# Kernel tuning notes

Measured on AMD Instinct MI355X. Metric: run time of the kernel, lower is better.

Reference implementation:

```python
import jax, jax.numpy as jnp
import numpy as np

EPS = 1e-5  # BatchNorm eps (torch default)


def setup_inputs() -> dict:
    key = jax.random.key(0)
    ks = jax.random.split(key, 12)
    B, T, F = 2048, 128, 84

    def rn(k, sh, scale=0.05):
        return jax.random.normal(k, sh, jnp.float32) * scale

    return {
        "x": jax.random.normal(ks[0], (B, T, F), jnp.float32),
        # Conv1d(84 -> 64, k=3, pad=1)
        "conv1d_w": rn(ks[1], (64, F, 3)),
        "conv1d_b": rn(ks[2], (64,)),
        # BatchNorm1d(64), eval mode (running stats)
        "bn_gamma": jnp.ones((64,), jnp.float32),
        "bn_beta": jnp.zeros((64,), jnp.float32),
        "bn_mean": jnp.zeros((64,), jnp.float32),
        "bn_var": jnp.ones((64,), jnp.float32),
        # Linear(64*16 -> 64*4*4)
        "lin_w": rn(ks[3], (1024, 1024)),
        "lin_b": rn(ks[4], (1024,)),
        # ConvLSTM cell: Conv2d(192 -> 512, k=3, pad=1, groups=4)
        "cell_w": rn(ks[5], (512, 48, 3, 3)),
        "cell_b": rn(ks[6], (512,)),
        # Classifier
        "cls1_w": rn(ks[7], (128, 2048)),
        "cls1_b": rn(ks[8], (128,)),
        "cls2_w": rn(ks[9], (2, 128)),
        "cls2_b": rn(ks[10], (2,)),
    }


def reference(x, conv1d_w, conv1d_b, bn_gamma, bn_beta, bn_mean, bn_var,
              lin_w, lin_b, cell_w, cell_b, cls1_w, cls1_b, cls2_w, cls2_b):
    B, T, F = x.shape
    H = 128  # hidden channels

    # Per-timestep encoder is state-free -> vectorize over (B, T).
    # Conv1d k=3 pad=1 on a length-1 sequence: only the center tap hits data.
    enc = jnp.einsum('btf,cf->btc', x, conv1d_w[:, :, 1]) + conv1d_b  # [B,T,64]
    enc = (enc - bn_mean) * (bn_gamma / jnp.sqrt(bn_var + EPS)) + bn_beta
    enc = jax.nn.relu(enc)
    # flatten of [64,16] is channel-major -> repeat along last axis.
    flat = jnp.repeat(enc, 16, axis=-1)                               # [B,T,1024]
    to2d = jnp.einsum('btk,ok->bto', flat, lin_w) + lin_b             # [B,T,1024]
    xt = to2d.reshape(B, T, 64, 4, 4).transpose(1, 0, 2, 3, 4)        # [T,B,64,4,4]

    def step(carry, x_t):
        h, c = carry
        comb = jnp.concatenate([x_t, h], axis=1)                      # [B,192,4,4]
        conv = jax.lax.conv_general_dilated(
            comb, cell_w, window_strides=(1, 1), padding='SAME',
            dimension_numbers=('NCHW', 'OIHW', 'NCHW'),
            feature_group_count=4)
        conv = conv + cell_b[None, :, None, None]                     # [B,512,4,4]
        cc_i, cc_f, cc_o, cc_g = jnp.split(conv, 4, axis=1)
        c_next = jax.nn.sigmoid(cc_f) * c + jax.nn.sigmoid(cc_i) * jnp.tanh(cc_g)
        h_next = jax.nn.sigmoid(cc_o) * jnp.tanh(c_next)
        return (h_next, c_next), None

    h0 = jnp.zeros((B, H, 4, 4), x.dtype)
    (h_last, _), _ = jax.lax.scan(step, (h0, h0), xt)

    feat = h_last.reshape(B, H * 16)                                  # [B,2048]
    hid = jax.nn.relu(feat @ cls1_w.T + cls1_b)
    return hid @ cls2_w.T + cls2_b                                    # [B,2]
```

## Files before the change

kernel.cpp:

```cpp
#include <hip/hip_runtime.h>
#include <math.h>

#define BN_EPS 1e-5f

typedef _Float16 f16x8 __attribute__((ext_vector_type(8)));
typedef _Float16 f16x4 __attribute__((ext_vector_type(4)));
typedef _Float16 f16x2 __attribute__((ext_vector_type(2)));
typedef unsigned short u16x8 __attribute__((ext_vector_type(8)));
typedef float f32x4 __attribute__((ext_vector_type(4)));
typedef float f32x16 __attribute__((ext_vector_type(16)));


__global__ void prep_enc_w(const float* __restrict__ conv1d_w,
                           const float* __restrict__ conv1d_b,
                           const float* __restrict__ gamma,
                           const float* __restrict__ beta,
                           const float* __restrict__ mean,
                           const float* __restrict__ var,
                           float* __restrict__ We, float* __restrict__ be) {
  int tid = blockIdx.x * blockDim.x + threadIdx.x;
  if (tid < 5376) {
    int c = tid / 84, f = tid % 84;
    float s = gamma[c] * rsqrtf(var[c] + BN_EPS);
    We[c * 84 + f] = s * conv1d_w[c * 252 + f * 3 + 1];
    if (f == 0) be[c] = s * conv1d_b[c] + (beta[c] - mean[c] * s);
  }
}

__global__ void prep_wef(const float* __restrict__ We, _Float16* __restrict__ WeF) {
  int tid = blockIdx.x * blockDim.x + threadIdx.x;
  if (tid >= 6144) return;
  int j = tid & 7, lane = (tid >> 3) & 63, kch = (tid >> 9) % 3, ct = tid / 1536;
  int c = ct * 16 + (lane & 15);
  int k = kch * 32 + (lane >> 4) * 8 + j;
  WeF[tid] = (k < 84) ? (_Float16)We[c * 84 + k] : (_Float16)0.f;
}

__global__ void prep_w2(const float* __restrict__ lin_w, float* __restrict__ W2) {
  int tid = blockIdx.x * blockDim.x + threadIdx.x;
  int o2 = tid >> 6, c = tid & 63;
  float s = 0.f;
#pragma unroll
  for (int j = 0; j < 16; ++j) s += lin_w[o2 * 1024 + c * 16 + j];
  W2[o2 * 64 + c] = s;
}

__global__ void prep_A(const float* __restrict__ cell_w,
                       const float* __restrict__ cell_b,
                       const float* __restrict__ lin_b,
                       const float* __restrict__ W2,
                       float* __restrict__ A, float* __restrict__ Abias) {
  int tid = blockIdx.x * blockDim.x + threadIdx.x;
  int go = tid >> 10;
  int c = (tid >> 4) & 63;
  int p = tid & 15;
  int y = p >> 2, x = p & 3;
  int kn = (go >= 128) ? 16 : 48;
  int xb = (go >= 128) ? 48 : 0;
  float a = 0.f;
  for (int k = 0; k < kn; ++k)
    for (int dy = 0; dy < 3; ++dy) {
      int yy = y + dy - 1;
      if (yy < 0 || yy > 3) continue;
      for (int dx = 0; dx < 3; ++dx) {
        int xx = x + dx - 1;
        if (xx < 0 || xx > 3) continue;
        a += cell_w[((go * 48 + k) * 3 + dy) * 3 + dx] *
             W2[((xb + k) * 16 + yy * 4 + xx) * 64 + c];
      }
    }
  A[(go * 64 + c) * 16 + p] = a;
  if (c == 0) {
    float bs = cell_b[go];
    for (int k = 0; k < kn; ++k)
      for (int dy = 0; dy < 3; ++dy) {
        int yy = y + dy - 1;
        if (yy < 0 || yy > 3) continue;
        for (int dx = 0; dx < 3; ++dx) {
          int xx = x + dx - 1;
          if (xx < 0 || xx > 3) continue;
          bs += cell_w[((go * 48 + k) * 3 + dy) * 3 + dx] *
                lin_b[(xb + k) * 16 + yy * 4 + xx];
        }
      }
    Abias[go * 16 + p] = bs;
  }
}

__global__ void pack_a16(const float* __restrict__ A, _Float16* __restrict__ Apk) {
  int tid = blockIdx.x * blockDim.x + threadIdx.x;
  int j = tid & 7, lane = (tid >> 3) & 63, kch = (tid >> 9) & 1, go = tid >> 10;
  int p = lane & 15;
  int c = kch * 32 + (lane >> 4) * 8 + j;
  Apk[tid] = (_Float16)A[(go * 64 + c) * 16 + p];
}

__global__ void pack_wcv(const float* __restrict__ cell_w, _Float16* __restrict__ Wcv) {
  int tid = blockIdx.x * blockDim.x + threadIdx.x;
  int j = tid & 7, lane = (tid >> 3) & 63, m = (tid >> 9) & 3, tmk = tid >> 11;
  int co = m * 32 + (lane & 31);
  int khi = (lane >> 5) * 8 + j;
  float v;
  if (tmk < 18) {
    int kch = tmk / 9, tap = tmk % 9;
    v = cell_w[((size_t)(128 + co) * 48 + 16 + kch * 16 + khi) * 9 + tap];
  } else if (tmk < 45) {
    int r = tmk - 18; int kch = r / 9, tap = r % 9;
    v = cell_w[((size_t)(256 + co) * 48 + kch * 16 + khi) * 9 + tap];
  } else {
    int r = tmk - 45; int kch = r / 9, tap = r % 9;
    v = cell_w[((size_t)(384 + co) * 48 + kch * 16 + khi) * 9 + tap];
  }
  Wcv[tid] = (_Float16)v;
}

__device__ __forceinline__ float sigm(float v) {
  return __fdividef(1.f, 1.f + __expf(-v));
}
__device__ __forceinline__ float tanh_fast(float v) {
  return 1.f - __fdividef(2.f, __expf(2.f * v) + 1.f);
}

__global__ __launch_bounds__(256, 3) void xgate_kernel(
    const float* __restrict__ x, const _Float16* __restrict__ WeF,
    const float* __restrict__ be, const _Float16* __restrict__ Apk,
    const float* __restrict__ Abias, unsigned short* __restrict__ sixf, int tc) {
  __shared__ __align__(16) _Float16 x16[128 * 104];
  __shared__ __align__(16) _Float16 enc_s[128 * 72];
  __shared__ __align__(16) unsigned char Tt[4 * 2304];
  int tid = threadIdx.x, lane = tid & 63, w = tid >> 6;
  int gq = blockIdx.x >> 7, cq = blockIdx.x & 127;
  int n = lane & 15, kgrp = lane >> 4;

  {
    int r = tid >> 1, half = tid & 1;
    int b = cq * 16 + (r >> 3), t = tc * 8 + (r & 7);
    const float* rowp = x + ((size_t)b * 128 + t) * 84;
#pragma unroll
    for (int j = 0; j < 11; ++j) {
      int q = half + 2 * j;
      if (q < 21) {
        float4 v = *(const float4*)(rowp + q * 4);
        f16x4 h;
        h[0] = (_Float16)v.x; h[1] = (_Float16)v.y;
        h[2] = (_Float16)v.z; h[3] = (_Float16)v.w;
        *(f16x4*)(&x16[r * 104 + q * 4]) = h;
      }
    }
    for (int i = tid; i < 4096; i += 256) {
      int rr = i >> 5, k = i & 31;
      if (k < 20) x16[rr * 104 + 84 + k] = (_Float16)0.f;
    }
  }
  __syncthreads();

  for (int ct4 = 0; ct4 < 8; ++ct4) {
    f32x4 acc = *(const f32x4*)(be + w * 16 + kgrp * 4);
#pragma unroll
    for (int kch = 0; kch < 3; ++kch)
      acc = __builtin_amdgcn_mfma_f32_16x16x32_f16(
          *(const f16x8*)(WeF + ((w * 3 + kch) * 64 + lane) * 8),
          *(const f16x8*)(&x16[(ct4 * 16 + n) * 104 + kch * 32 + kgrp * 8]),
          acc, 0, 0, 0);
#pragma unroll
    for (int r = 0; r < 4; ++r)
      enc_s[(ct4 * 16 + n) * 72 + w * 16 + kgrp * 4 + r] =
          (_Float16)fmaxf(acc[r], 0.f);
  }
  __syncthreads();

  int slotB = gq >> 1;
  int chbase = (gq & 1) * 64 + w * 16;
  unsigned char* Tw = Tt + w * 2304;
  int fn = lane >> 2;
  for (int ct4 = 0; ct4 < 8; ++ct4) {
    int ccl = ct4 * 16 + n;
    int fb = cq * 16 + ct4 * 2 + (fn >> 3), ftr = fn & 7;
    size_t grow =
        (((size_t)fb * 8 + ftr) * 2 + slotB) * 2048 + (size_t)chbase * 16;
    for (int gb = 0; gb < 4; ++gb) {
#pragma unroll
      for (int gi = 0; gi < 4; ++gi) {
        int gol = gb * 4 + gi;
        int go = gq * 64 + w * 16 + gol;
        f32x4 acc = *(const f32x4*)(Abias + go * 16 + kgrp * 4);
        acc = __builtin_amdgcn_mfma_f32_16x16x32_f16(
            *(const f16x8*)(Apk + (size_t)go * 1024 + lane * 8),
            *(const f16x8*)(&enc_s[ccl * 72 + kgrp * 8]), acc, 0, 0, 0);
        acc = __builtin_amdgcn_mfma_f32_16x16x32_f16(
            *(const f16x8*)(Apk + (size_t)go * 1024 + 512 + lane * 8),
            *(const f16x8*)(&enc_s[ccl * 72 + 32 + kgrp * 8]), acc, 0, 0, 0);
        unsigned char* tdst = Tw + n * 144 + gi * 32 + kgrp * 8;
        if (gq < 2) {
#pragma unroll
          for (int rp = 0; rp < 2; ++rp) {
            unsigned lo = (unsigned)(sigm(acc[rp * 2]) * 65535.f + 0.5f);
            unsigned hi = (unsigned)(sigm(acc[rp * 2 + 1]) * 65535.f + 0.5f);
            *(unsigned*)(tdst + rp * 4) = lo | (hi << 16);
          }
        } else {
#pragma unroll
          for (int rp = 0; rp < 2; ++rp) {
            f16x2 pv = {(_Float16)acc[rp * 2], (_Float16)acc[rp * 2 + 1]};
            *(f16x2*)(tdst + rp * 4) = pv;
          }
        }
      }
      asm volatile("s_waitcnt lgkmcnt(0)" ::: "memory");
      __builtin_amdgcn_sched_barrier(0);
#pragma unroll
      for (int j = 0; j < 2; ++j) {
        int chunk = (lane & 3) + 4 * j;
        f16x8 v = *(const f16x8*)(Tw + fn * 144 + chunk * 16);
        *(f16x8*)(sixf + grow + (size_t)gb * 64 + (size_t)chunk * 8) = v;
      }
      asm volatile("s_waitcnt lgkmcnt(0)" ::: "memory");
      __builtin_amdgcn_sched_barrier(0);
    }
  }
}

#define HPB 4624
#define HPQ 272
#define ZQ 4352
#define COFF 36992
#define GOFF 102528
#define GSZ 18432
#define CBOFF 157824
#define LDSZ 158848

__device__ __forceinline__ void update_items(
    unsigned char* lds, const unsigned short* __restrict__ sixf_b,
    _Float16* __restrict__ h16_b, int tid, int q) {
  int tP = q >> 2, hfP = (q >> 1) & 1, ntP = q & 1;
  bool lastT = (tP == 7);
  float* cbase = (float*)(lds + COFF) + (hfP * 2 + ntP) * 4096;
#pragma unroll 2
  for (int k = 0; k < 6; ++k) {
    int item = tid + k * 768;
    if (item < 4096) {
      int cell = item >> 4, p = item & 15;
      int ch = cell & 127, blbit = cell >> 7;
      int b = hfP * 4 + ntP * 2 + blbit;
      const unsigned short* sp =
          sixf_b + ((size_t)b * 8 + tP) * 4096 + ch * 16 + p;
      float si = (float)sp[0] * (1.f / 65535.f);
      float xf = (float)*(const _Float16*)(sp + 2048);
      unsigned gbyte = (unsigned)(ch * 144 + ntP * 64 + blbit * 32 + p * 2);
      float gf = (float)*(const _Float16*)(lds + GOFF + 0 * GSZ + gbyte);
      float go = (float)*(const _Float16*)(lds + GOFF + 1 * GSZ + gbyte);
      float gg = (float)*(const _Float16*)(lds + GOFF + 2 * GSZ + gbyte);
      float cbo = *(const float*)(lds + CBOFF + ch * 4);
      float cbg = *(const float*)(lds + CBOFF + 512 + ch * 4);
      float* cp = cbase + cell * 16 + p;
      float cv = sigm(xf + gf) * cp[0] + si * tanh_fast(cbg + gg);
      cp[0] = cv;
      float hn = sigm(cbo + go) * tanh_fast(cv);
      *(_Float16*)(lds + b * HPB + p * HPQ + ch * 2) = (_Float16)hn;
      if (lastT) h16_b[((size_t)b * 16 + p) * 128 + ch] = (_Float16)hn;
    }
  }
}

template <int GATE>
__device__ __forceinline__ void role_loop(
    unsigned char* lds, const _Float16* __restrict__ Wg,
    const unsigned short* __restrict__ sixf_b,
    _Float16* __restrict__ h16_b,
    int m, int lane, int tid, const unsigned* tapbase, unsigned gwbase) {
  constexpr int NKCH = (GATE == 0) ? 2 : 3;
  constexpr unsigned CIOFF = (GATE == 0) ? 0u : (GATE == 1 ? 64u : 160u);
  f16x8 wr[NKCH * 9];
#pragma unroll
  for (int fi = 0; fi < NKCH * 9; ++fi)
    wr[fi] = *(const f16x8*)(Wg + (size_t)(fi * 4 + m) * 512 + (lane << 3));

  for (int q = 0; q < 32; ++q) {
    if (q > 0) update_items(lds, sixf_b, h16_b, tid, q - 1);
    int hf = (q >> 1) & 1, nt = q & 1;
    unsigned bofs = (unsigned)(hf * 4 + nt * 2) * HPB;
    f32x16 acc = {};
#pragma unroll
    for (int kch = 0; kch < NKCH; ++kch)
#pragma unroll
      for (int tap = 0; tap < 9; ++tap)
        acc = __builtin_amdgcn_mfma_f32_32x32x16_f16(
            wr[kch * 9 + tap],
            *(const f16x8*)(lds + tapbase[tap] + bofs + CIOFF +
                            (unsigned)kch * 32),
            acc, 0, 0, 0);
#pragma unroll
    for (int r = 0; r < 16; ++r) {
      unsigned co_l = (unsigned)((r & 3) + 8 * (r >> 2));
      *(_Float16*)(lds + gwbase + (unsigned)GATE * GSZ + co_l * 144u +
                   (unsigned)nt * 64u) = (_Float16)acc[r];
    }
    __syncthreads();
  }
  update_items(lds, sixf_b, h16_b, tid, 31);
  __syncthreads();
}

__global__ __launch_bounds__(768, 3) void recur8_kernel(
    const unsigned short* __restrict__ sixf, const _Float16* __restrict__ Wcv,
    const float* __restrict__ cell_b, _Float16* __restrict__ h16,
    float* __restrict__ cstate) {
  __shared__ __align__(16) unsigned char lds[LDSZ];
  int tid = threadIdx.x, lane = tid & 63, w = tid >> 6;
  int gate = w >> 2, m = w & 3;

  _Float16* h16_b = h16 + (size_t)blockIdx.x * 16384;
  for (int i = tid; i < 16384; i += 768) {
    int bl8 = i >> 11, q = (i >> 7) & 15, chh = i & 127;
    *(_Float16*)(lds + bl8 * HPB + q * HPQ + chh * 2) = h16_b[i];
  }
  for (int i = tid; i < 1024; i += 768) {
    int bl8 = i >> 7, chh = i & 127;
    *(_Float16*)(lds + bl8 * HPB + ZQ + chh * 2) = (_Float16)0.f;
  }
  float* cl = (float*)(lds + COFF);
  float* cst_b = cstate + (size_t)blockIdx.x * 16384;
  for (int i = tid; i < 16384; i += 768) cl[i] = cst_b[i];
  if (tid < 256) *(float*)(lds + CBOFF + tid * 4) = cell_b[256 + tid];

  int col = lane & 31, khalf = lane >> 5, b_lo = col >> 4, p_c = col & 15;
  int yc = p_c >> 2, xc = p_c & 3;
  unsigned tapbase[9];
#pragma unroll
  for (int dy = 0; dy < 3; ++dy)
#pragma unroll
    for (int dx = 0; dx < 3; ++dx) {
      int qy = yc + dy - 1, qx = xc + dx - 1;
      bool valid = (qy >= 0 && qy < 4 && qx >= 0 && qx < 4);
      tapbase[dy * 3 + dx] =
          (valid ? (unsigned)((qy * 4 + qx) * HPQ) : (unsigned)ZQ) +
          (unsigned)(b_lo * HPB + khalf * 16);
    }
  unsigned gwbase = (unsigned)GOFF + (unsigned)((m * 32 + khalf * 4) * 144) +
                    (unsigned)(b_lo * 32 + p_c * 2);
  __syncthreads();

  const unsigned short* sixf_b = sixf + (size_t)blockIdx.x * 262144;
  if (gate == 0)
    role_loop<0>(lds, Wcv, sixf_b, h16_b, m, lane, tid, tapbase, gwbase);
  else if (gate == 1)
    role_loop<1>(lds, Wcv + 36864, sixf_b, h16_b, m, lane, tid, tapbase, gwbase);
  else
    role_loop<2>(lds, Wcv + 92160, sixf_b, h16_b, m, lane, tid, tapbase, gwbase);

  for (int i = tid; i < 16384; i += 768) cst_b[i] = cl[i];
}

__global__ __launch_bounds__(128) void cls_kernel(
    const _Float16* __restrict__ h16, const float* __restrict__ w1,
    const float* __restrict__ b1, const float* __restrict__ w2,
    const float* __restrict__ b2, float* __restrict__ out) {
  __shared__ __align__(16) float feat[8 * 2064];
  __shared__ float hid[8 * 128];
  int b0 = blockIdx.x * 8;
  for (int i = threadIdx.x; i < 16384; i += 128) {
    int bl = i >> 11, r = i & 2047, p = r >> 7, chh = r & 127;
    feat[bl * 2064 + chh * 16 + p] = (float)h16[(size_t)b0 * 2048 + i];
  }
  __syncthreads();
  int ch = threadIdx.x;
  float acc[8];
#pragma unroll
  for (int b = 0; b < 8; ++b) acc[b] = b1[ch];
  const float4* wr = (const float4*)(w1 + (size_t)ch * 2048);
  for (int k4 = 0; k4 < 512; ++k4) {
    float4 wv = wr[k4];
#pragma unroll
    for (int b = 0; b < 8; ++b) {
      float4 f = *(const float4*)(&feat[b * 2064 + k4 * 4]);
      acc[b] += wv.x * f.x + wv.y * f.y + wv.z * f.z + wv.w * f.w;
    }
  }
#pragma unroll
  for (int b = 0; b < 8; ++b) hid[b * 128 + ch] = fmaxf(acc[b], 0.f);
  __syncthreads();
  if (threadIdx.x < 16) {
    int b = threadIdx.x >> 1, o = threadIdx.x & 1;
    float s = b2[o];
    for (int k = 0; k < 128; ++k) s += hid[b * 128 + k] * w2[o * 128 + k];
    out[(size_t)(b0 + b) * 2 + o] = s;
  }
}

extern "C" void kernel_launch(void* const* d_in, const int* in_sizes, int n_in,
                              void* d_out, int out_size, void* d_ws, size_t ws_size,
                              hipStream_t stream) {
  const float* x        = (const float*)d_in[0];
  const float* conv1d_w = (const float*)d_in[1];
  const float* conv1d_b = (const float*)d_in[2];
  const float* bn_gamma = (const float*)d_in[3];
  const float* bn_beta  = (const float*)d_in[4];
  const float* bn_mean  = (const float*)d_in[5];
  const float* bn_var   = (const float*)d_in[6];
  const float* lin_w    = (const float*)d_in[7];
  const float* lin_b    = (const float*)d_in[8];
  const float* cell_w   = (const float*)d_in[9];
  const float* cell_b   = (const float*)d_in[10];
  const float* cls1_w   = (const float*)d_in[11];
  const float* cls1_b   = (const float*)d_in[12];
  const float* cls2_w   = (const float*)d_in[13];
  const float* cls2_b   = (const float*)d_in[14];

  float* ws = (float*)d_ws;
  float* We    = ws + 0;
  float* be    = ws + 8192;
  float* W2    = ws + 12288;
  float* A     = ws + 81920;
  float* Abias = ws + 344064;
  _Float16* WeF = (_Float16*)(ws + 348160);
  _Float16* Apk = (_Float16*)(ws + 352256);
  _Float16* Wcv = (_Float16*)(ws + 483328);
  _Float16* h16 = (_Float16*)(ws + 557056);
  float* cstate = ws + 2654208;
  unsigned short* sixf = (unsigned short*)(ws + 6848512);
  float* out = (float*)d_out;

  prep_enc_w<<<21, 256, 0, stream>>>(conv1d_w, conv1d_b, bn_gamma, bn_beta,
                                     bn_mean, bn_var, We, be);
  prep_wef<<<24, 256, 0, stream>>>(We, WeF);
  prep_w2<<<256, 256, 0, stream>>>(lin_w, W2);
  prep_A<<<1024, 256, 0, stream>>>(cell_w, cell_b, lin_b, W2, A, Abias);
  pack_a16<<<1024, 256, 0, stream>>>(A, Apk);
  pack_wcv<<<576, 256, 0, stream>>>(cell_w, Wcv);
  hipMemsetAsync(h16, 0, 8388608, stream);
  hipMemsetAsync(cstate, 0, 16777216, stream);
  for (int tc = 0; tc < 16; ++tc) {
    xgate_kernel<<<512, 256, 0, stream>>>(x, WeF, be, Apk, Abias, sixf, tc);
    recur8_kernel<<<256, 768, 0, stream>>>(sixf, Wcv, cell_b, h16, cstate);
  }
  cls_kernel<<<256, 128, 0, stream>>>(h16, cls1_w, cls1_b, cls2_w, cls2_b, out);
}
```

Baseline: 3.651 ms.

## Vectorize LSTM cell update and assign fixed per-thread update tasks by warp role

Replaces the strided per-element gate update loop with a per-thread task that processes 8 spatial positions using 16-byte vector loads from global and LDS. Each thread keeps a fixed channel/batch-bit/half assignment, and the cell biases live in registers instead of LDS. The work is split across the gate roles: gate-0 warps update every step, while gate-1 and gate-2 warps alternate by tile parity. This cuts the address arithmetic, scalar loads and bias LDS traffic in the update phase. In exchange, the update work is spread unevenly across the warp roles and register pressure rises.

```diff
diff --git a/kernel.cpp b/kernel.cpp
--- a/kernel.cpp
+++ b/kernel.cpp
@@ -226,39 +226,35 @@
 #define COFF 36992
 #define GOFF 102528
 #define GSZ 18432
-#define CBOFF 157824
-#define LDSZ 158848
-
-__device__ __forceinline__ void update_items(
+#define LDSZ 157824
+
+__device__ __forceinline__ void vupdate(
     unsigned char* lds, const unsigned short* __restrict__ sixf_b,
-    _Float16* __restrict__ h16_b, int tid, int q) {
+    _Float16* __restrict__ h16_b, int ch, int blbit, int h8,
+    float cbo, float cbg, int q) {
   int tP = q >> 2, hfP = (q >> 1) & 1, ntP = q & 1;
+  int b = hfP * 4 + ntP * 2 + blbit;
   bool lastT = (tP == 7);
-  float* cbase = (float*)(lds + COFF) + (hfP * 2 + ntP) * 4096;
-#pragma unroll 2
-  for (int k = 0; k < 6; ++k) {
-    int item = tid + k * 768;
-    if (item < 4096) {
-      int cell = item >> 4, p = item & 15;
-      int ch = cell & 127, blbit = cell >> 7;
-      int b = hfP * 4 + ntP * 2 + blbit;
-      const unsigned short* sp =
-          sixf_b + ((size_t)b * 8 + tP) * 4096 + ch * 16 + p;
-      float si = (float)sp[0] * (1.f / 65535.f);
-      float xf = (float)*(const _Float16*)(sp + 2048);
-      unsigned gbyte = (unsigned)(ch * 144 + ntP * 64 + blbit * 32 + p * 2);
-      float gf = (float)*(const _Float16*)(lds + GOFF + 0 * GSZ + gbyte);
-      float go = (float)*(const _Float16*)(lds + GOFF + 1 * GSZ + gbyte);
-      float gg = (float)*(const _Float16*)(lds + GOFF + 2 * GSZ + gbyte);
-      float cbo = *(const float*)(lds + CBOFF + ch * 4);
-      float cbg = *(const float*)(lds + CBOFF + 512 + ch * 4);
-      float* cp = cbase + cell * 16 + p;
-      float cv = sigm(xf + gf) * cp[0] + si * tanh_fast(cbg + gg);
-      cp[0] = cv;
-      float hn = sigm(cbo + go) * tanh_fast(cv);
-      *(_Float16*)(lds + b * HPB + p * HPQ + ch * 2) = (_Float16)hn;
-      if (lastT) h16_b[((size_t)b * 16 + p) * 128 + ch] = (_Float16)hn;
-    }
+  const unsigned short* sp =
+      sixf_b + ((size_t)b * 8 + tP) * 4096 + ch * 16 + h8 * 8;
+  u16x8 s = *(const u16x8*)sp;
+  f16x8 xv = *(const f16x8*)(sp + 2048);
+  unsigned gbyte = (unsigned)(ch * 144 + ntP * 64 + blbit * 32 + h8 * 16);
+  f16x8 gfv = *(const f16x8*)(lds + GOFF + 0 * GSZ + gbyte);
+  f16x8 gov = *(const f16x8*)(lds + GOFF + 1 * GSZ + gbyte);
+  f16x8 ggv = *(const f16x8*)(lds + GOFF + 2 * GSZ + gbyte);
+  float* cp = (float*)(lds + COFF) +
+              (((hfP * 2 + ntP) * 256 + blbit * 128 + ch) * 16 + h8 * 8);
+#pragma unroll
+  for (int j = 0; j < 8; ++j) {
+    int p = h8 * 8 + j;
+    float si = (float)s[j] * (1.f / 65535.f);
+    float cv = sigm((float)xv[j] + (float)gfv[j]) * cp[j] +
+               si * tanh_fast(cbg + (float)ggv[j]);
+    cp[j] = cv;
+    float hn = sigm(cbo + (float)gov[j]) * tanh_fast(cv);
+    *(_Float16*)(lds + b * HPB + p * HPQ + ch * 2) = (_Float16)hn;
+    if (lastT) h16_b[((size_t)b * 16 + p) * 128 + ch] = (_Float16)hn;
   }
 }
 
@@ -267,7 +263,8 @@
     unsigned char* lds, const _Float16* __restrict__ Wg,
     const unsigned short* __restrict__ sixf_b,
     _Float16* __restrict__ h16_b,
-    int m, int lane, int tid, const unsigned* tapbase, unsigned gwbase) {
+    int m, int lane, int tid, const unsigned* tapbase, unsigned gwbase,
+    int ch_u, int blbit_u, int h8_u, float cbo, float cbg) {
   constexpr int NKCH = (GATE == 0) ? 2 : 3;
   constexpr unsigned CIOFF = (GATE == 0) ? 0u : (GATE == 1 ? 64u : 160u);
   f16x8 wr[NKCH * 9];
@@ -276,7 +273,12 @@
     wr[fi] = *(const f16x8*)(Wg + (size_t)(fi * 4 + m) * 512 + (lane << 3));
 
   for (int q = 0; q < 32; ++q) {
-    if (q > 0) update_items(lds, sixf_b, h16_b, tid, q - 1);
+    if (q > 0) {
+      int ntP = (q - 1) & 1;
+      bool own = (GATE == 0) || (GATE == 1 && ntP == 0) || (GATE == 2 && ntP == 1);
+      if (own)
+        vupdate(lds, sixf_b, h16_b, ch_u, blbit_u, h8_u, cbo, cbg, q - 1);
+    }
     int hf = (q >> 1) & 1, nt = q & 1;
     unsigned bofs = (unsigned)(hf * 4 + nt * 2) * HPB;
     f32x16 acc = {};
@@ -297,7 +299,8 @@
     }
     __syncthreads();
   }
-  update_items(lds, sixf_b, h16_b, tid, 31);
+  if (GATE == 0 || GATE == 2)
+    vupdate(lds, sixf_b, h16_b, ch_u, blbit_u, h8_u, cbo, cbg, 31);
   __syncthreads();
 }
 
@@ -321,7 +324,10 @@
   float* cl = (float*)(lds + COFF);
   float* cst_b = cstate + (size_t)blockIdx.x * 16384;
   for (int i = tid; i < 16384; i += 768) cl[i] = cst_b[i];
-  if (tid < 256) *(float*)(lds + CBOFF + tid * 4) = cell_b[256 + tid];
+
+  int task = (gate == 2) ? (tid - 256) : tid;
+  int ch_u = task >> 2, blbit_u = (task >> 1) & 1, h8_u = task & 1;
+  float cbo = cell_b[256 + ch_u], cbg = cell_b[384 + ch_u];
 
   int col = lane & 31, khalf = lane >> 5, b_lo = col >> 4, p_c = col & 15;
   int yc = p_c >> 2, xc = p_c & 3;
@@ -342,11 +348,14 @@
 
   const unsigned short* sixf_b = sixf + (size_t)blockIdx.x * 262144;
   if (gate == 0)
-    role_loop<0>(lds, Wcv, sixf_b, h16_b, m, lane, tid, tapbase, gwbase);
+    role_loop<0>(lds, Wcv, sixf_b, h16_b, m, lane, tid, tapbase, gwbase,
+                 ch_u, blbit_u, h8_u, cbo, cbg);
   else if (gate == 1)
-    role_loop<1>(lds, Wcv + 36864, sixf_b, h16_b, m, lane, tid, tapbase, gwbase);
+    role_loop<1>(lds, Wcv + 36864, sixf_b, h16_b, m, lane, tid, tapbase, gwbase,
+                 ch_u, blbit_u, h8_u, cbo, cbg);
   else
-    role_loop<2>(lds, Wcv + 92160, sixf_b, h16_b, m, lane, tid, tapbase, gwbase);
+    role_loop<2>(lds, Wcv + 92160, sixf_b, h16_b, m, lane, tid, tapbase, gwbase,
+                 ch_u, blbit_u, h8_u, cbo, cbg);
 
   for (int i = tid; i < 16384; i += 768) cst_b[i] = cl[i];
 }
```

Result: no change. 3.593 ms (-1.6%).
